# Kernel tuning notes

Hardware: AMD Instinct MI355X
Metric: run time of the kernel (lower is better)

The kernel has to match this reference:

```python
import jax, jax.numpy as jnp
import numpy as np
from jax import lax

H = W = 512
NT = 1000


def setup_inputs() -> dict:
    key = jax.random.key(0)
    kx, ky = jax.random.split(key)
    X = jax.random.uniform(kx, (H, W), dtype=jnp.float32)
    Y = jax.random.uniform(ky, (H, W), dtype=jnp.float32)
    return {"X": X, "Y": Y}


def reference(X, Y):
    # Gaussian initial condition, same math as torch.exp(-50*((X-0.5)^2+(Y-0.5)^2))
    x0 = jnp.exp(-50.0 * ((X - 0.5) ** 2 + (Y - 0.5) ** 2))
    h, w = x0.shape
    # mask zeroing the boundary (rows/cols 0 and -1)
    mask = jnp.zeros((h, w), dtype=x0.dtype).at[1:-1, 1:-1].set(1.0)

    def step(x, _):
        # 3x3 cross kernel [[0,.25,0],[.25,0,.25],[0,.25,0]] with zero padding=1,
        # expressed as four shifted adds (identical math, no conv launch overhead)
        p = jnp.pad(x, 1)
        xn = 0.25 * (p[:-2, 1:-1] + p[2:, 1:-1] + p[1:-1, :-2] + p[1:-1, 2:])
        return xn * mask, None

    x, _ = lax.scan(step, x0, None, length=NT)
    # original returns NCHW with N=C=1
    return x[None, None]
```

## Files before the change

kernel.cpp:

```cpp
#include <hip/hip_runtime.h>
#include <math.h>


#define HW 512
#define NP 128

__device__ __forceinline__ int mode_of(int p) {
    return (p < 64) ? (p + 1) : (p + 383);
}

__device__ __forceinline__ float gauss(const float* __restrict__ X,
                                       const float* __restrict__ Y, int idx) {
    float dx = X[idx] - 0.5f, dy = Y[idx] - 0.5f;
    return expf(-50.0f * (dx * dx + dy * dy));
}

__global__ void k_prep(const float* __restrict__ X, const float* __restrict__ Y,
                       float* __restrict__ x1, float* __restrict__ S,
                       float* __restrict__ ST, float* __restrict__ L,
                       float* __restrict__ C1, float* __restrict__ D) {
    int b = blockIdx.x, t = threadIdx.x;
    if (b < 1024) {
        int idx = b * 256 + t;
        int i = idx >> 9, j = idx & 511;
        float v = 0.0f;
        if (i > 0 && i < HW - 1 && j > 0 && j < HW - 1) {
            v = 0.25f * (gauss(X, Y, idx - HW) + gauss(X, Y, idx + HW) +
                         gauss(X, Y, idx - 1)  + gauss(X, Y, idx + 1));
        }
        x1[idx] = v;
    } else if (b < 1280) {
        int idx = (b - 1024) * 256 + t;
        int p = idx >> 9, i = idx & 511;
        long tt = ((long)mode_of(p) * (long)i) % 1022;
        S[idx] = (float)sin((double)tt * (M_PI / 511.0));
    } else if (b < 1536) {
        int idx = (b - 1280) * 256 + t;
        int i = idx >> 7, p = idx & 127;
        long tt = ((long)mode_of(p) * (long)i) % 1022;
        ST[idx] = (float)sin((double)tt * (M_PI / 511.0));
    } else if (b < 1600) {
        int idx = (b - 1536) * 256 + t;
        int p = idx >> 7, q = idx & 127;
        double lp = cos((double)mode_of(p) * M_PI / 511.0);
        double lq = cos((double)mode_of(q) * M_PI / 511.0);
        double lam = 0.5 * (lp + lq);
        double mag = pow(fabs(lam), 999.0);
        if (lam < 0.0) mag = -mag;
        L[idx] = (float)(mag * (2.0 / 511.0) * (2.0 / 511.0));
    } else if (b < 1664) {
        ((float4*)C1)[(b - 1600) * 256 + t] = float4{0.f, 0.f, 0.f, 0.f};
    } else {
        ((float4*)D)[(b - 1664) * 256 + t] = float4{0.f, 0.f, 0.f, 0.f};
    }
}

__global__ void k_m1(const float* __restrict__ S, const float* __restrict__ x1,
                     float* __restrict__ C1) {
    int j = blockIdx.x * 256 + threadIdx.x;
    int p0 = blockIdx.y * 2;
    int i0 = blockIdx.z * 128;
    const float* S0 = S + p0 * HW + i0;
    const float* S1 = S0 + HW;
    const float* xp = x1 + i0 * HW + j;
    float a0 = 0.f, a1 = 0.f;
    #pragma unroll 8
    for (int i = 0; i < 128; i++) {
        float x = xp[i * HW];
        a0 += S0[i] * x;
        a1 += S1[i] * x;
    }
    unsafeAtomicAdd(&C1[p0 * HW + j], a0);
    unsafeAtomicAdd(&C1[(p0 + 1) * HW + j], a1);
}

__global__ void k_m2(const float* __restrict__ C1, const float* __restrict__ ST,
                     const float* __restrict__ L, float* __restrict__ D) {
    __shared__ float c1[64];
    int p = blockIdx.x, jc = blockIdx.y, q = threadIdx.x;
    if (q < 64) c1[q] = C1[p * HW + jc * 64 + q];
    __syncthreads();
    const float* STp = ST + jc * 64 * NP + q;
    float acc = 0.f;
    #pragma unroll 8
    for (int j = 0; j < 64; j++) acc += c1[j] * STp[j * NP];
    unsafeAtomicAdd(&D[p * NP + q], acc * L[p * NP + q]);
}

__global__ void k_m3(const float* __restrict__ D, const float* __restrict__ S,
                     float* __restrict__ E) {
    __shared__ float drow[NP];
    int j = blockIdx.x * 256 + threadIdx.x;
    int p = blockIdx.y;
    if (threadIdx.x < NP) drow[threadIdx.x] = D[p * NP + threadIdx.x];
    __syncthreads();
    float acc = 0.f;
    #pragma unroll 8
    for (int q = 0; q < NP; q++) acc += drow[q] * S[q * HW + j];
    E[p * HW + j] = acc;
}

__global__ void k_m4(const float* __restrict__ S, const float* __restrict__ E,
                     float* __restrict__ out) {
    int j = blockIdx.x * 256 + threadIdx.x;
    int i0 = blockIdx.y * 2;
    float a0 = 0.f, a1 = 0.f;
    #pragma unroll 8
    for (int p = 0; p < NP; p++) {
        float e = E[p * HW + j];
        a0 += S[p * HW + i0] * e;
        a1 += S[p * HW + i0 + 1] * e;
    }
    out[(i0 + 0) * HW + j] = a0;
    out[(i0 + 1) * HW + j] = a1;
}


extern "C" void kernel_launch(void* const* d_in, const int* in_sizes, int n_in,
                              void* d_out, int out_size, void* d_ws, size_t ws_size,
                              hipStream_t stream) {
    const float* X = (const float*)d_in[0];
    const float* Y = (const float*)d_in[1];
    float* out = (float*)d_out;

    float* ws = (float*)d_ws;
    float* x1 = ws;
    float* S  = x1 + HW * HW;
    float* ST = S + NP * HW;
    float* L  = ST + HW * NP;
    float* C1 = L + NP * NP;
    float* D  = C1 + NP * HW;
    float* E  = D + NP * NP;

    k_prep<<<dim3(1680),        dim3(256), 0, stream>>>(X, Y, x1, S, ST, L, C1, D);
    k_m1  <<<dim3(2, 64, 4),    dim3(256), 0, stream>>>(S, x1, C1);
    k_m2  <<<dim3(NP, 8),       dim3(128), 0, stream>>>(C1, ST, L, D);
    k_m3  <<<dim3(2, NP),       dim3(256), 0, stream>>>(D, S, E);
    k_m4  <<<dim3(2, 256),      dim3(256), 0, stream>>>(S, E, out);
}
```

Measured before the change: 87.76 us.

## Fuse spectral middle matmuls into one kernel and widen per-thread tiles

Merges the second and third spectral projection kernels into a single per-mode kernel that keeps the C1 row and the scaled D row in shared memory. This removes the D buffer, its zeroing and its atomics, plus one launch. The first and last matmul kernels now compute four output rows per thread instead of two, so each x1/E load is reused more often. In exchange the fused kernel runs only 128 blocks of 128 threads, which may underuse the GPU.

```diff
diff --git a/kernel.cpp b/kernel.cpp
--- a/kernel.cpp
+++ b/kernel.cpp
@@ -18,7 +18,7 @@
 __global__ void k_prep(const float* __restrict__ X, const float* __restrict__ Y,
                        float* __restrict__ x1, float* __restrict__ S,
                        float* __restrict__ ST, float* __restrict__ L,
-                       float* __restrict__ C1, float* __restrict__ D) {
+                       float* __restrict__ C1) {
     int b = blockIdx.x, t = threadIdx.x;
     if (b < 1024) {
         int idx = b * 256 + t;
@@ -48,71 +48,88 @@
         double mag = pow(fabs(lam), 999.0);
         if (lam < 0.0) mag = -mag;
         L[idx] = (float)(mag * (2.0 / 511.0) * (2.0 / 511.0));
-    } else if (b < 1664) {
+    } else {
         ((float4*)C1)[(b - 1600) * 256 + t] = float4{0.f, 0.f, 0.f, 0.f};
-    } else {
-        ((float4*)D)[(b - 1664) * 256 + t] = float4{0.f, 0.f, 0.f, 0.f};
     }
 }
 
 __global__ void k_m1(const float* __restrict__ S, const float* __restrict__ x1,
                      float* __restrict__ C1) {
     int j = blockIdx.x * 256 + threadIdx.x;
-    int p0 = blockIdx.y * 2;
-    int i0 = blockIdx.z * 128;
+    int p0 = blockIdx.y * 4;
+    int i0 = blockIdx.z * 64;
     const float* S0 = S + p0 * HW + i0;
     const float* S1 = S0 + HW;
+    const float* S2 = S1 + HW;
+    const float* S3 = S2 + HW;
     const float* xp = x1 + i0 * HW + j;
-    float a0 = 0.f, a1 = 0.f;
+    float a0 = 0.f, a1 = 0.f, a2 = 0.f, a3 = 0.f;
     #pragma unroll 8
-    for (int i = 0; i < 128; i++) {
+    for (int i = 0; i < 64; i++) {
         float x = xp[i * HW];
         a0 += S0[i] * x;
         a1 += S1[i] * x;
+        a2 += S2[i] * x;
+        a3 += S3[i] * x;
     }
-    unsafeAtomicAdd(&C1[p0 * HW + j], a0);
+    unsafeAtomicAdd(&C1[(p0 + 0) * HW + j], a0);
     unsafeAtomicAdd(&C1[(p0 + 1) * HW + j], a1);
+    unsafeAtomicAdd(&C1[(p0 + 2) * HW + j], a2);
+    unsafeAtomicAdd(&C1[(p0 + 3) * HW + j], a3);
 }
 
-__global__ void k_m2(const float* __restrict__ C1, const float* __restrict__ ST,
-                     const float* __restrict__ L, float* __restrict__ D) {
-    __shared__ float c1[64];
-    int p = blockIdx.x, jc = blockIdx.y, q = threadIdx.x;
-    if (q < 64) c1[q] = C1[p * HW + jc * 64 + q];
+__global__ void k_m23(const float* __restrict__ C1, const float* __restrict__ ST,
+                      const float* __restrict__ L, const float* __restrict__ S,
+                      float* __restrict__ E) {
+    __shared__ float c1[HW];
+    __shared__ float drow[NP];
+    int p = blockIdx.x, t = threadIdx.x;
+    #pragma unroll
+    for (int k = 0; k < 4; k++) c1[t + k * NP] = C1[p * HW + t + k * NP];
     __syncthreads();
-    const float* STp = ST + jc * 64 * NP + q;
-    float acc = 0.f;
+    float b0 = 0.f, b1 = 0.f, b2 = 0.f, b3 = 0.f;
     #pragma unroll 8
-    for (int j = 0; j < 64; j++) acc += c1[j] * STp[j * NP];
-    unsafeAtomicAdd(&D[p * NP + q], acc * L[p * NP + q]);
-}
-
-__global__ void k_m3(const float* __restrict__ D, const float* __restrict__ S,
-                     float* __restrict__ E) {
-    __shared__ float drow[NP];
-    int j = blockIdx.x * 256 + threadIdx.x;
-    int p = blockIdx.y;
-    if (threadIdx.x < NP) drow[threadIdx.x] = D[p * NP + threadIdx.x];
+    for (int j = 0; j < HW; j += 4) {
+        b0 += c1[j + 0] * ST[(j + 0) * NP + t];
+        b1 += c1[j + 1] * ST[(j + 1) * NP + t];
+        b2 += c1[j + 2] * ST[(j + 2) * NP + t];
+        b3 += c1[j + 3] * ST[(j + 3) * NP + t];
+    }
+    drow[t] = ((b0 + b1) + (b2 + b3)) * L[p * NP + t];
     __syncthreads();
-    float acc = 0.f;
+    float e0 = 0.f, e1 = 0.f, e2 = 0.f, e3 = 0.f;
     #pragma unroll 8
-    for (int q = 0; q < NP; q++) acc += drow[q] * S[q * HW + j];
-    E[p * HW + j] = acc;
+    for (int q = 0; q < NP; q++) {
+        float d = drow[q];
+        const float* Sq = S + q * HW + t;
+        e0 += d * Sq[0];
+        e1 += d * Sq[128];
+        e2 += d * Sq[256];
+        e3 += d * Sq[384];
+    }
+    E[p * HW + t + 0]   = e0;
+    E[p * HW + t + 128] = e1;
+    E[p * HW + t + 256] = e2;
+    E[p * HW + t + 384] = e3;
 }
 
 __global__ void k_m4(const float* __restrict__ S, const float* __restrict__ E,
                      float* __restrict__ out) {
     int j = blockIdx.x * 256 + threadIdx.x;
-    int i0 = blockIdx.y * 2;
-    float a0 = 0.f, a1 = 0.f;
-    #pragma unroll 8
+    int i0 = blockIdx.y * 4;
+    float a0 = 0.f, a1 = 0.f, a2 = 0.f, a3 = 0.f;
+    #pragma unroll 16
     for (int p = 0; p < NP; p++) {
         float e = E[p * HW + j];
-        a0 += S[p * HW + i0] * e;
+        a0 += S[p * HW + i0 + 0] * e;
         a1 += S[p * HW + i0 + 1] * e;
+        a2 += S[p * HW + i0 + 2] * e;
+        a3 += S[p * HW + i0 + 3] * e;
     }
     out[(i0 + 0) * HW + j] = a0;
     out[(i0 + 1) * HW + j] = a1;
+    out[(i0 + 2) * HW + j] = a2;
+    out[(i0 + 3) * HW + j] = a3;
 }
 
 
@@ -129,12 +146,10 @@
     float* ST = S + NP * HW;
     float* L  = ST + HW * NP;
     float* C1 = L + NP * NP;
-    float* D  = C1 + NP * HW;
-    float* E  = D + NP * NP;
+    float* E  = C1 + NP * HW;
 
-    k_prep<<<dim3(1680),        dim3(256), 0, stream>>>(X, Y, x1, S, ST, L, C1, D);
-    k_m1  <<<dim3(2, 64, 4),    dim3(256), 0, stream>>>(S, x1, C1);
-    k_m2  <<<dim3(NP, 8),       dim3(128), 0, stream>>>(C1, ST, L, D);
-    k_m3  <<<dim3(2, NP),       dim3(256), 0, stream>>>(D, S, E);
-    k_m4  <<<dim3(2, 256),      dim3(256), 0, stream>>>(S, E, out);
+    k_prep<<<dim3(1664),        dim3(256), 0, stream>>>(X, Y, x1, S, ST, L, C1);
+    k_m1  <<<dim3(2, 32, 8),    dim3(256), 0, stream>>>(S, x1, C1);
+    k_m23 <<<dim3(NP),          dim3(128), 0, stream>>>(C1, ST, L, S, E);
+    k_m4  <<<dim3(2, 128),      dim3(256), 0, stream>>>(S, E, out);
 }
```

Measured after the change: 85.85 us. 2.2% less time.
